# Performance work log

Measured on AMD Instinct MI355X. Metric: run time of the kernel, lower is better.

Reference implementation:

```python
import jax, jax.numpy as jnp
import numpy as np

B, S, E, H = 1, 2048, 512, 8
D = E // H
N = B * S
WIN_HALF = 32  # attention_window 64 -> +/-32
ALPHA = 0.1
LN_EPS = 1e-12
NEG_INF = -1e9


def _build_window_edges():
    # windowed graph: dst i attends to src j with |i-j| <= WIN_HALF, within each batch block
    i = np.arange(S)
    offs = np.arange(-WIN_HALF, WIN_HALF + 1)
    src = i[:, None] + offs[None, :]
    dst = np.broadcast_to(i[:, None], src.shape)
    valid = (src >= 0) & (src < S)
    src, dst = src[valid], dst[valid]
    srcs, dsts = [], []
    for b in range(B):
        srcs.append(src + b * S)
        dsts.append(dst + b * S)
    return (np.concatenate(srcs).astype(np.int32),
            np.concatenate(dsts).astype(np.int32))


def setup_inputs() -> dict:
    key = jax.random.key(0)
    ks = jax.random.split(key, 12)
    sc = 1.0 / np.sqrt(E)
    src_np, dst_np = _build_window_edges()
    return {
        "hidden_states": jax.random.normal(ks[0], (B, S, E), dtype=jnp.float32),
        "attention_mask": jnp.zeros((B, S), dtype=jnp.float32),
        "edge_src": jnp.asarray(src_np),
        "edge_dst": jnp.asarray(dst_np),
        "Wq": jax.random.normal(ks[1], (E, E), dtype=jnp.float32) * sc,
        "bq": jnp.zeros((E,), dtype=jnp.float32),
        "Wk": jax.random.normal(ks[2], (E, E), dtype=jnp.float32) * sc,
        "bk": jnp.zeros((E,), dtype=jnp.float32),
        "Wv": jax.random.normal(ks[3], (E, E), dtype=jnp.float32) * sc,
        "bv": jnp.zeros((E,), dtype=jnp.float32),
        "Wo": jax.random.normal(ks[4], (E, E), dtype=jnp.float32) * sc,
        "bo": jnp.zeros((E,), dtype=jnp.float32),
        "ln_g": jnp.ones((E,), dtype=jnp.float32),
        "ln_b": jnp.zeros((E,), dtype=jnp.float32),
    }


def reference(hidden_states, attention_mask, edge_src, edge_dst,
              Wq, bq, Wk, bk, Wv, bv, Wo, bo, ln_g, ln_b):
    x = hidden_states  # (B,S,E); node ordering n = b*S + s (matches torch reshape)
    q = ((x @ Wq + bq) / jnp.sqrt(jnp.asarray(D, x.dtype))).reshape(N, H, D)
    k = (x @ Wk + bk).reshape(N, H, D)
    v = (x @ Wv + bv).reshape(N, H, D)

    mask = (attention_mask >= 0).reshape(N)  # bool per node

    # u_dot_v('k','q','score'): per-edge, per-head dot product
    score = jnp.einsum('ehd,ehd->eh', k[edge_src], q[edge_dst])  # (Eg,H)
    score = jnp.where(mask[edge_src][:, None], score, NEG_INF)

    # edge_softmax over incoming edges of each destination node
    smax = jax.ops.segment_max(score, edge_dst, num_segments=N)
    p = jnp.exp(score - smax[edge_dst])
    denom = jax.ops.segment_sum(p, edge_dst, num_segments=N)
    p = p / denom[edge_dst]  # (Eg,H)

    # 5 diffusion steps: h <- A h, blended with residual v (dropout off in eval)
    h = v
    for _ in range(5):
        m = h[edge_src] * p[:, :, None]                      # u_mul_e
        h = jax.ops.segment_sum(m, edge_dst, num_segments=N)  # sum('m','h')
        h = (1.0 - ALPHA) * h + ALPHA * v

    attn = h.reshape(B, S, E)

    # DiffuserSelfOutput: dense -> residual add -> LayerNorm
    y = attn @ Wo + bo + hidden_states
    mu = y.mean(-1, keepdims=True)
    var = ((y - mu) ** 2).mean(-1, keepdims=True)
    out = (y - mu) * jax.lax.rsqrt(var + LN_EPS) * ln_g + ln_b
    return out
```

## Files before the change

kernel.cpp:

```cpp
#include <hip/hip_runtime.h>
#include <math.h>

#define S_LEN 2048
#define E_DIM 512
#define NE (S_LEN * E_DIM)
#define H_NUM 8
#define WH 32
#define NOFF 65
#define PROW (H_NUM * NOFF)
#define PN (S_LEN * PROW)

typedef float f32x4 __attribute__((ext_vector_type(4)));
typedef short short8 __attribute__((ext_vector_type(8)));

__device__ __forceinline__ unsigned short f2bf(float f) {
    union { float f; unsigned u; } cv; cv.f = f;
    unsigned u = cv.u;
    u += 0x7fffu + ((u >> 16) & 1u);
    return (unsigned short)(u >> 16);
}
__device__ __forceinline__ unsigned pk2(float x, float y) {
    return (unsigned)f2bf(x) | ((unsigned)f2bf(y) << 16);
}

#define LGKM_BARRIER() do {                                   \
    __builtin_amdgcn_sched_barrier(0);                        \
    asm volatile("s_waitcnt lgkmcnt(0)" ::: "memory");        \
    __builtin_amdgcn_s_barrier();                             \
    __builtin_amdgcn_sched_barrier(0);                        \
} while (0)

__device__ __forceinline__ void mfma_gemm_f32(
    const float* __restrict__ A, const float* __restrict__ W,
    const float* __restrict__ bias, float* __restrict__ C,
    float scale, int m0, int n0)
{
    __shared__ unsigned short As[2][64 * 40];
    __shared__ unsigned short Bs[2][64 * 40];
    const int tid = threadIdx.x;
    const int lane = tid & 63, wave = tid >> 6;
    const int quad = lane >> 4, l16 = lane & 15;
    const int wr = (wave >> 1) * 32, wc = (wave & 1) * 32;
    const int ar = tid >> 2, ac = (tid & 3) * 8;
    const int bn = tid & 63, bk0 = (tid >> 6) * 8;

    f32x4 acc00 = {0.f,0.f,0.f,0.f}, acc01 = acc00, acc10 = acc00, acc11 = acc00;

    const float* Arow = A + (size_t)(m0 + ar) * E_DIM;

    float4 a0r[2], a1r[2];
    float  br[2][8];

#define QLOAD(s_, i_) do {                                                    \
        int kk_ = (i_) * 32;                                                  \
        a0r[s_] = *(const float4*)(Arow + kk_ + ac);                          \
        a1r[s_] = *(const float4*)(Arow + kk_ + ac + 4);                      \
        _Pragma("unroll")                                                     \
        for (int j_ = 0; j_ < 8; ++j_)                                        \
            br[s_][j_] = W[(size_t)(kk_ + bk0 + j_) * E_DIM + n0 + bn];       \
    } while (0)

#define QPACK(s_, b_) do {                                                    \
        uint4 ap_;                                                            \
        ap_.x = pk2(a0r[s_].x, a0r[s_].y); ap_.y = pk2(a0r[s_].z, a0r[s_].w); \
        ap_.z = pk2(a1r[s_].x, a1r[s_].y); ap_.w = pk2(a1r[s_].z, a1r[s_].w); \
        *(uint4*)(&As[b_][0] + ar * 40 + ac) = ap_;                           \
        uint4 bp_;                                                            \
        bp_.x = pk2(br[s_][0], br[s_][1]); bp_.y = pk2(br[s_][2], br[s_][3]); \
        bp_.z = pk2(br[s_][4], br[s_][5]); bp_.w = pk2(br[s_][6], br[s_][7]); \
        *(uint4*)(&Bs[b_][0] + bn * 40 + bk0) = bp_;                          \
    } while (0)

    QLOAD(0, 0);
    QPACK(0, 0);
    QLOAD(1, 1);
    LGKM_BARRIER();

#pragma unroll
    for (int it = 0; it < 16; ++it) {
        if (it < 14) QLOAD(it & 1, it + 2);

        const unsigned short* Ab = &As[it & 1][0];
        const unsigned short* Bb = &Bs[it & 1][0];
        short8 fa0 = *(const short8*)(Ab + (wr + l16) * 40 + quad * 8);
        short8 fa1 = *(const short8*)(Ab + (wr + 16 + l16) * 40 + quad * 8);
        short8 fb0 = *(const short8*)(Bb + (wc + l16) * 40 + quad * 8);
        short8 fb1 = *(const short8*)(Bb + (wc + 16 + l16) * 40 + quad * 8);
        acc00 = __builtin_amdgcn_mfma_f32_16x16x32_bf16(fa0, fb0, acc00, 0, 0, 0);
        acc01 = __builtin_amdgcn_mfma_f32_16x16x32_bf16(fa0, fb1, acc01, 0, 0, 0);
        acc10 = __builtin_amdgcn_mfma_f32_16x16x32_bf16(fa1, fb0, acc10, 0, 0, 0);
        acc11 = __builtin_amdgcn_mfma_f32_16x16x32_bf16(fa1, fb1, acc11, 0, 0, 0);

        if (it < 15) {
            QPACK((it + 1) & 1, (it + 1) & 1);
            LGKM_BARRIER();
        }
    }
#undef QLOAD
#undef QPACK

#pragma unroll
    for (int mi = 0; mi < 2; ++mi) {
#pragma unroll
        for (int ni = 0; ni < 2; ++ni) {
            f32x4 a = (mi == 0) ? ((ni == 0) ? acc00 : acc01)
                                : ((ni == 0) ? acc10 : acc11);
            int n = n0 + wc + ni * 16 + l16;
            float bval = bias[n];
#pragma unroll
            for (int r = 0; r < 4; ++r) {
                int m = m0 + wr + mi * 16 + quad * 4 + r;
                C[(size_t)m * E_DIM + n] = (a[r] + bval) * scale;
            }
        }
    }
}

__global__ __launch_bounds__(256)
void qkv_gemm(const float* __restrict__ x,
              const float* __restrict__ Wq, const float* __restrict__ bq,
              const float* __restrict__ Wk, const float* __restrict__ bk,
              const float* __restrict__ Wv, const float* __restrict__ bv,
              float* __restrict__ q, float* __restrict__ k, float* __restrict__ v)
{
    const float* W; const float* b; float* o; float sc;
    if (blockIdx.z == 0)      { W = Wq; b = bq; o = q; sc = 0.125f; }
    else if (blockIdx.z == 1) { W = Wk; b = bk; o = k; sc = 1.0f; }
    else                      { W = Wv; b = bv; o = v; sc = 1.0f; }
    mfma_gemm_f32(x, W, b, o, sc, blockIdx.y * 64, blockIdx.x * 64);
}

#define SDN 32
__global__ __launch_bounds__(256)
void scores_d1(const float* __restrict__ q, const float* __restrict__ k,
               const float* __restrict__ v, const float* __restrict__ amask,
               unsigned short* __restrict__ Pb, unsigned short* __restrict__ hAb)
{
    const int i0 = blockIdx.x * SDN;
    const int h  = blockIdx.y;
    const int tid = threadIdx.x;
    __shared__ float ks[96 * 68];
    __shared__ float am[96];
    __shared__ float ps[SDN * NOFF];

    for (int e = tid; e < 96 * 16; e += 256) {
        int lr = e >> 4, c4 = e & 15;
        int j = i0 - WH + lr;
        int jc = min(max(j, 0), S_LEN - 1);
        *(float4*)(ks + lr * 68 + c4 * 4) =
            *(const float4*)(k + (size_t)jc * E_DIM + h * 64 + c4 * 4);
    }
    if (tid < 96) {
        int j = i0 - WH + tid;
        am[tid] = (j >= 0 && j < S_LEN) ? amask[j] : -1.0f;
    }

    const int dst = tid >> 3;
    const int og  = tid & 7;
    float4 qreg[16];
    {
        const float4* qrow = (const float4*)(q + (size_t)(i0 + dst) * E_DIM + h * 64);
#pragma unroll
        for (int t = 0; t < 16; ++t) qreg[t] = qrow[t];
    }
    __syncthreads();

    float sreg[9];
#pragma unroll
    for (int t = 0; t < 9; ++t) sreg[t] = -INFINITY;
#pragma unroll
    for (int t = 0; t < 9; ++t) {
        int off = og + 8 * t;
        if (off > 64) break;
        int j = i0 + dst + off - WH;
        if (j >= 0 && j < S_LEN) {
            int lr = dst + off;
            const float4* kr = (const float4*)(ks + lr * 68);
            float acc = 0.f;
#pragma unroll
            for (int u = 0; u < 16; ++u) {
                float4 a = qreg[u], bb = kr[u];
                acc += a.x * bb.x + a.y * bb.y + a.z * bb.z + a.w * bb.w;
            }
            sreg[t] = (am[lr] >= 0.f) ? acc : -1e9f;
        }
    }
    __syncthreads();

    for (int e = tid; e < 96 * 16; e += 256) {
        int lr = e >> 4, c4 = e & 15;
        int j = i0 - WH + lr;
        int jc = min(max(j, 0), S_LEN - 1);
        *(float4*)(ks + lr * 68 + c4 * 4) =
            *(const float4*)(v + (size_t)jc * E_DIM + h * 64 + c4 * 4);
    }

    float mx = sreg[0];
#pragma unroll
    for (int t = 1; t < 9; ++t) mx = fmaxf(mx, sreg[t]);
#pragma unroll
    for (int o = 1; o < 8; o <<= 1) mx = fmaxf(mx, __shfl_xor(mx, o, 64));
    float dn = 0.f;
#pragma unroll
    for (int t = 0; t < 9; ++t) {
        sreg[t] = expf(sreg[t] - mx);
        dn += sreg[t];
    }
#pragma unroll
    for (int o = 1; o < 8; o <<= 1) dn += __shfl_xor(dn, o, 64);
    float rinv = 1.f / dn;
#pragma unroll
    for (int t = 0; t < 9; ++t) {
        int off = og + 8 * t;
        if (off > 64) break;
        float pv = sreg[t] * rinv;
        Pb[(size_t)(i0 + dst) * PROW + h * NOFF + off] = f2bf(pv);
        ps[dst * NOFF + off] = pv;
    }
    __syncthreads();

    {
        const int ci = tid & 15;
        const int ob = (tid >> 4) * 2;
        float4 a0 = {0,0,0,0}, a1 = a0;
        for (int lr = ob; lr < ob + 66; ++lr) {
            float4 hval = *(const float4*)(ks + lr * 68 + ci * 4);
            int o0 = lr - ob;
            if (o0 <= 64) {
                float p = ps[ob * NOFF + o0];
                a0.x += p * hval.x; a0.y += p * hval.y; a0.z += p * hval.z; a0.w += p * hval.w;
            }
            int o1 = o0 - 1;
            if ((unsigned)o1 <= 64u) {
                float p = ps[(ob + 1) * NOFF + o1];
                a1.x += p * hval.x; a1.y += p * hval.y; a1.z += p * hval.z; a1.w += p * hval.w;
            }
        }
#pragma unroll
        for (int r = 0; r < 2; ++r) {
            float4 a = r ? a1 : a0;
            float4 vv = *(const float4*)(ks + (WH + ob + r) * 68 + ci * 4);
            ushort4 o4;
            o4.x = f2bf(0.9f * a.x + 0.1f * vv.x);
            o4.y = f2bf(0.9f * a.y + 0.1f * vv.y);
            o4.z = f2bf(0.9f * a.z + 0.1f * vv.z);
            o4.w = f2bf(0.9f * a.w + 0.1f * vv.w);
            *(ushort4*)(hAb + (size_t)(i0 + ob + r) * E_DIM + h * 64 + ci * 4) = o4;
        }
    }
}

__global__ __launch_bounds__(512)
void diffuse4m(const unsigned short* __restrict__ hAb, const float* __restrict__ v,
               const unsigned short* __restrict__ Pb, unsigned short* __restrict__ h5b)
{
    __shared__ unsigned short inT[64 * 328];
    __shared__ unsigned short m1T[64 * 264];
    __shared__ unsigned short ps2[256 * 136];
    unsigned short* m2T = inT;
    unsigned short* m3T = m1T;
    const int i0 = blockIdx.x * 64;
    const int h  = blockIdx.y;
    const int c0 = h * 64;
    const int tid  = threadIdx.x;
    const int lane = tid & 63, wave = tid >> 6;
    const int quad = lane >> 4, l16 = lane & 15;

    for (int e = tid; e < 256 * 68; e += 512)
        ((unsigned*)ps2)[e] = 0u;

    for (int e = tid; e < 160 * 16; e += 512) {
        int rp = (e >> 4) * 2, c4 = (e & 15) * 4;
        int ja = min(max(i0 - 128 + rp,     0), S_LEN - 1);
        int jb = min(max(i0 - 128 + rp + 1, 0), S_LEN - 1);
        ushort4 ha = *(const ushort4*)(hAb + (size_t)ja * E_DIM + c0 + c4);
        ushort4 hb = *(const ushort4*)(hAb + (size_t)jb * E_DIM + c0 + c4);
        *(unsigned*)(inT + (c4 + 0) * 328 + rp) = (unsigned)ha.x | ((unsigned)hb.x << 16);
        *(unsigned*)(inT + (c4 + 1) * 328 + rp) = (unsigned)ha.y | ((unsigned)hb.y << 16);
        *(unsigned*)(inT + (c4 + 2) * 328 + rp) = (unsigned)ha.z | ((unsigned)hb.z << 16);
        *(unsigned*)(inT + (c4 + 3) * 328 + rp) = (unsigned)ha.w | ((unsigned)hb.w << 16);
    }
    __syncthreads();

    for (int it = 0; it < 32; ++it) {
        int row = wave + it * 8;
        int jc = min(max(i0 - 96 + row, 0), S_LEN - 1);
        const unsigned short* src = Pb + (size_t)jc * PROW + h * NOFF;
        unsigned short* dst = ps2 + row * 136 + 32 + (row & 7);
        dst[lane] = src[lane];
        if (lane == 0) dst[64] = src[64];
    }
    __syncthreads();

#define BAND_FA(roff_)                                                        \
    *(const short8*)(ps2 + (size_t)(m + (roff_)) * 136 + 32 +                 \
                     ((m + (roff_)) & 7) + (k0q - m))

#pragma unroll
    for (int uu = 0; uu < 4; ++uu) {
        int u = wave + uu * 8;
        int mtb = (u >> 1) * 16;
        int ntb = (u & 1) * 32;
        f32x4 a0 = {0.f,0.f,0.f,0.f}, a1 = a0;
        int ks0 = mtb >> 5;
        const int m = mtb + l16;
#pragma unroll
        for (int t = 0; t < 3; ++t) {
            int k0q = (ks0 + t) * 32 + quad * 8;
            short8 fa = BAND_FA(0);
            short8 fb0 = *(const short8*)(inT + (ntb + l16) * 328 + k0q);
            short8 fb1 = *(const short8*)(inT + (ntb + 16 + l16) * 328 + k0q);
            a0 = __builtin_amdgcn_mfma_f32_16x16x32_bf16(fa, fb0, a0, 0, 0, 0);
            a1 = __builtin_amdgcn_mfma_f32_16x16x32_bf16(fa, fb1, a1, 0, 0, 0);
        }
#pragma unroll
        for (int nt = 0; nt < 2; ++nt) {
            f32x4 a = nt ? a1 : a0;
            int n = ntb + nt * 16 + l16;
            float o[4];
#pragma unroll
            for (int r = 0; r < 4; ++r) {
                int gm = min(max(i0 - 96 + mtb + quad * 4 + r, 0), S_LEN - 1);
                o[r] = 0.9f * a[r] + 0.1f * v[(size_t)gm * E_DIM + c0 + n];
            }
            *(unsigned*)(m1T + n * 264 + mtb + quad * 4)     = pk2(o[0], o[1]);
            *(unsigned*)(m1T + n * 264 + mtb + quad * 4 + 2) = pk2(o[2], o[3]);
        }
    }
    __syncthreads();

#pragma unroll
    for (int uu = 0; uu < 3; ++uu) {
        int u = wave + uu * 8;
        int mtb = (u >> 1) * 16;
        int ntb = (u & 1) * 32;
        f32x4 a0 = {0.f,0.f,0.f,0.f}, a1 = a0;
        int ks0 = mtb >> 5;
        const int m = mtb + l16;
#pragma unroll
        for (int t = 0; t < 3; ++t) {
            int k0q = (ks0 + t) * 32 + quad * 8;
            short8 fa = BAND_FA(32);
            short8 fb0 = *(const short8*)(m1T + (ntb + l16) * 264 + k0q);
            short8 fb1 = *(const short8*)(m1T + (ntb + 16 + l16) * 264 + k0q);
            a0 = __builtin_amdgcn_mfma_f32_16x16x32_bf16(fa, fb0, a0, 0, 0, 0);
            a1 = __builtin_amdgcn_mfma_f32_16x16x32_bf16(fa, fb1, a1, 0, 0, 0);
        }
#pragma unroll
        for (int nt = 0; nt < 2; ++nt) {
            f32x4 a = nt ? a1 : a0;
            int n = ntb + nt * 16 + l16;
            float o[4];
#pragma unroll
            for (int r = 0; r < 4; ++r) {
                int gm = min(max(i0 - 64 + mtb + quad * 4 + r, 0), S_LEN - 1);
                o[r] = 0.9f * a[r] + 0.1f * v[(size_t)gm * E_DIM + c0 + n];
            }
            *(unsigned*)(m2T + n * 200 + mtb + quad * 4)     = pk2(o[0], o[1]);
            *(unsigned*)(m2T + n * 200 + mtb + quad * 4 + 2) = pk2(o[2], o[3]);
        }
    }
    __syncthreads();

#pragma unroll
    for (int uu = 0; uu < 2; ++uu) {
        int u = wave + uu * 8;
        int mtb = (u >> 1) * 16;
        int ntb = (u & 1) * 32;
        f32x4 a0 = {0.f,0.f,0.f,0.f}, a1 = a0;
        int ks0 = mtb >> 5;
        const int m = mtb + l16;
#pragma unroll
        for (int t = 0; t < 3; ++t) {
            int k0q = (ks0 + t) * 32 + quad * 8;
            short8 fa = BAND_FA(64);
            short8 fb0 = *(const short8*)(m2T + (ntb + l16) * 200 + k0q);
            short8 fb1 = *(const short8*)(m2T + (ntb + 16 + l16) * 200 + k0q);
            a0 = __builtin_amdgcn_mfma_f32_16x16x32_bf16(fa, fb0, a0, 0, 0, 0);
            a1 = __builtin_amdgcn_mfma_f32_16x16x32_bf16(fa, fb1, a1, 0, 0, 0);
        }
#pragma unroll
        for (int nt = 0; nt < 2; ++nt) {
            f32x4 a = nt ? a1 : a0;
            int n = ntb + nt * 16 + l16;
            float o[4];
#pragma unroll
            for (int r = 0; r < 4; ++r) {
                int gm = min(max(i0 - 32 + mtb + quad * 4 + r, 0), S_LEN - 1);
                o[r] = 0.9f * a[r] + 0.1f * v[(size_t)gm * E_DIM + c0 + n];
            }
            *(unsigned*)(m3T + n * 136 + mtb + quad * 4)     = pk2(o[0], o[1]);
            *(unsigned*)(m3T + n * 136 + mtb + quad * 4 + 2) = pk2(o[2], o[3]);
        }
    }
    __syncthreads();

    {
        int u = wave;
        int mtb = (u >> 1) * 16;
        int ntb = (u & 1) * 32;
        f32x4 a0 = {0.f,0.f,0.f,0.f}, a1 = a0;
        int ks0 = mtb >> 5;
        const int m = mtb + l16;
#pragma unroll
        for (int t = 0; t < 3; ++t) {
            int k0q = (ks0 + t) * 32 + quad * 8;
            short8 fa = BAND_FA(96);
            short8 fb0 = *(const short8*)(m3T + (ntb + l16) * 136 + k0q);
            short8 fb1 = *(const short8*)(m3T + (ntb + 16 + l16) * 136 + k0q);
            a0 = __builtin_amdgcn_mfma_f32_16x16x32_bf16(fa, fb0, a0, 0, 0, 0);
            a1 = __builtin_amdgcn_mfma_f32_16x16x32_bf16(fa, fb1, a1, 0, 0, 0);
        }
#pragma unroll
        for (int nt = 0; nt < 2; ++nt) {
            f32x4 a = nt ? a1 : a0;
            int n = ntb + nt * 16 + l16;
#pragma unroll
            for (int r = 0; r < 4; ++r) {
                int gm = i0 + mtb + quad * 4 + r;
                float vv = v[(size_t)gm * E_DIM + c0 + n];
                h5b[(size_t)gm * E_DIM + c0 + n] = f2bf(0.9f * a[r] + 0.1f * vv);
            }
        }
    }
#undef BAND_FA
}

__global__ __launch_bounds__(512)
void oln5(const unsigned short* __restrict__ h5b, const float* __restrict__ Wo,
          const float* __restrict__ bo, const float* __restrict__ x,
          const float* __restrict__ g, const float* __restrict__ lb,
          float* __restrict__ out)
{
    __shared__ unsigned short Bs2[2][512 * 40];
    __shared__ float rsum[8][16], rsq[8][16];
    const int tid = threadIdx.x;
    const int lane = tid & 63, wave = tid >> 6;
    const int quad = lane >> 4, l16 = lane & 15;
    const int m0 = blockIdx.x * 16;
    const int n = tid;

    short8 far_[16];
#pragma unroll
    for (int t = 0; t < 16; ++t)
        far_[t] = *(const short8*)(h5b + (size_t)(m0 + l16) * E_DIM + t * 32 + quad * 8);

    {
        float w0[32];
#pragma unroll
        for (int j = 0; j < 32; ++j)
            w0[j] = Wo[(size_t)j * E_DIM + n];
#pragma unroll
        for (int t = 0; t < 4; ++t) {
            uint4 bp;
            bp.x = pk2(w0[t*8+0], w0[t*8+1]); bp.y = pk2(w0[t*8+2], w0[t*8+3]);
            bp.z = pk2(w0[t*8+4], w0[t*8+5]); bp.w = pk2(w0[t*8+6], w0[t*8+7]);
            *(uint4*)(&Bs2[0][0] + n * 40 + t * 8) = bp;
        }
    }
    LGKM_BARRIER();

    f32x4 acc[4];
#pragma unroll
    for (int t = 0; t < 4; ++t) acc[t] = (f32x4){0.f,0.f,0.f,0.f};

#pragma unroll
    for (int it = 0; it < 16; ++it) {
        float wn[32];
        if (it < 15) {
#pragma unroll
            for (int j = 0; j < 32; ++j)
                wn[j] = Wo[(size_t)((it + 1) * 32 + j) * E_DIM + n];
        }

#pragma unroll
        for (int nt = 0; nt < 4; ++nt) {
            short8 fb = *(const short8*)(&Bs2[it & 1][0] +
                                         (wave * 64 + nt * 16 + l16) * 40 + quad * 8);
            acc[nt] = __builtin_amdgcn_mfma_f32_16x16x32_bf16(far_[it], fb, acc[nt], 0, 0, 0);
        }

        if (it < 15) {
#pragma unroll
            for (int t = 0; t < 4; ++t) {
                uint4 bp;
                bp.x = pk2(wn[t*8+0], wn[t*8+1]); bp.y = pk2(wn[t*8+2], wn[t*8+3]);
                bp.z = pk2(wn[t*8+4], wn[t*8+5]); bp.w = pk2(wn[t*8+6], wn[t*8+7]);
                *(uint4*)(&Bs2[(it + 1) & 1][0] + n * 40 + t * 8) = bp;
            }
            LGKM_BARRIER();
        }
    }

    float s[4] = {0.f,0.f,0.f,0.f}, s2[4] = {0.f,0.f,0.f,0.f};
#pragma unroll
    for (int nt = 0; nt < 4; ++nt) {
        int nc = wave * 64 + nt * 16 + l16;
        float bv = bo[nc];
#pragma unroll
        for (int r = 0; r < 4; ++r) {
            int m = m0 + quad * 4 + r;
            float vl = acc[nt][r] + bv + x[(size_t)m * E_DIM + nc];
            acc[nt][r] = vl;
            s[r] += vl; s2[r] += vl * vl;
        }
    }
#pragma unroll
    for (int o = 1; o < 16; o <<= 1) {
#pragma unroll
        for (int r = 0; r < 4; ++r) {
            s[r]  += __shfl_xor(s[r], o, 64);
            s2[r] += __shfl_xor(s2[r], o, 64);
        }
    }
    if (l16 == 0) {
#pragma unroll
        for (int r = 0; r < 4; ++r) {
            rsum[wave][quad * 4 + r] = s[r];
            rsq[wave][quad * 4 + r]  = s2[r];
        }
    }
    __syncthreads();
    float mu[4], rs[4];
#pragma unroll
    for (int r = 0; r < 4; ++r) {
        int rl = quad * 4 + r;
        float tot = 0.f, tot2 = 0.f;
#pragma unroll
        for (int w = 0; w < 8; ++w) { tot += rsum[w][rl]; tot2 += rsq[w][rl]; }
        float m_ = tot * (1.f / 512.f);
        float var = tot2 * (1.f / 512.f) - m_ * m_;
        mu[r] = m_; rs[r] = rsqrtf(var + 1e-12f);
    }
#pragma unroll
    for (int nt = 0; nt < 4; ++nt) {
        int nc = wave * 64 + nt * 16 + l16;
        float gv = g[nc], bbv = lb[nc];
#pragma unroll
        for (int r = 0; r < 4; ++r) {
            int m = m0 + quad * 4 + r;
            out[(size_t)m * E_DIM + nc] = (acc[nt][r] - mu[r]) * rs[r] * gv + bbv;
        }
    }
}

extern "C" void kernel_launch(void* const* d_in, const int* in_sizes, int n_in,
                              void* d_out, int out_size, void* d_ws, size_t ws_size,
                              hipStream_t stream)
{
    const float* x     = (const float*)d_in[0];
    const float* amask = (const float*)d_in[1];
    const float* Wq = (const float*)d_in[4];
    const float* bq = (const float*)d_in[5];
    const float* Wk = (const float*)d_in[6];
    const float* bk = (const float*)d_in[7];
    const float* Wv = (const float*)d_in[8];
    const float* bv = (const float*)d_in[9];
    const float* Wo = (const float*)d_in[10];
    const float* bo = (const float*)d_in[11];
    const float* lng = (const float*)d_in[12];
    const float* lnb = (const float*)d_in[13];
    float* out = (float*)d_out;

    float* ws = (float*)d_ws;
    float* q  = ws;
    float* k  = ws + (size_t)NE;
    float* v  = ws + (size_t)2 * NE;
    unsigned short* Pb  = (unsigned short*)(ws + (size_t)3 * NE);
    unsigned short* hAb = Pb + (size_t)PN;
    unsigned short* h5b = hAb + (size_t)NE;

    qkv_gemm<<<dim3(8, 32, 3), 256, 0, stream>>>(x, Wq, bq, Wk, bk, Wv, bv, q, k, v);

    scores_d1<<<dim3(64, 8), 256, 0, stream>>>(q, k, v, amask, Pb, hAb);

    diffuse4m<<<dim3(32, 8), 512, 0, stream>>>(hAb, v, Pb, h5b);

    oln5<<<128, 512, 0, stream>>>(h5b, Wo, bo, x, lng, lnb, out);
}
```

Measured before the change: 155.1 us.

## Store V in bf16 and run first diffusion step on MFMA

The V projection is now written as bf16, which halves V traffic in the scores and diffusion kernels, and every consumer converts it back. The first diffusion step in scores_d1 moves from a scalar fp32 banded loop to bf16 MFMA. It uses a zero-padded, skewed bf16 probability tile and a transposed V tile in shared memory, so V is loaded up front and one barrier is removed. The cost is reduced precision of V and of step-1 probabilities, plus extra shared-memory setup.

```diff
diff --git a/kernel.cpp b/kernel.cpp
--- a/kernel.cpp
+++ b/kernel.cpp
@@ -22,6 +22,9 @@
 __device__ __forceinline__ unsigned pk2(float x, float y) {
     return (unsigned)f2bf(x) | ((unsigned)f2bf(y) << 16);
 }
+__device__ __forceinline__ float bf2f(unsigned short u) {
+    union { unsigned u; float f; } cv; cv.u = ((unsigned)u) << 16; return cv.f;
+}
 
 #define LGKM_BARRIER() do {                                   \
     __builtin_amdgcn_sched_barrier(0);                        \
@@ -33,7 +36,7 @@
 __device__ __forceinline__ void mfma_gemm_f32(
     const float* __restrict__ A, const float* __restrict__ W,
     const float* __restrict__ bias, float* __restrict__ C,
-    float scale, int m0, int n0)
+    unsigned short* __restrict__ Cb, float scale, int m0, int n0)
 {
     __shared__ unsigned short As[2][64 * 40];
     __shared__ unsigned short Bs[2][64 * 40];
@@ -110,7 +113,8 @@
 #pragma unroll
             for (int r = 0; r < 4; ++r) {
                 int m = m0 + wr + mi * 16 + quad * 4 + r;
-                C[(size_t)m * E_DIM + n] = (a[r] + bval) * scale;
+                if (Cb) Cb[(size_t)m * E_DIM + n] = f2bf((a[r] + bval) * scale);
+                else    C [(size_t)m * E_DIM + n] = (a[r] + bval) * scale;
             }
         }
     }
@@ -121,27 +125,35 @@
               const float* __restrict__ Wq, const float* __restrict__ bq,
               const float* __restrict__ Wk, const float* __restrict__ bk,
               const float* __restrict__ Wv, const float* __restrict__ bv,
-              float* __restrict__ q, float* __restrict__ k, float* __restrict__ v)
+              float* __restrict__ q, float* __restrict__ k,
+              unsigned short* __restrict__ vb)
 {
-    const float* W; const float* b; float* o; float sc;
-    if (blockIdx.z == 0)      { W = Wq; b = bq; o = q; sc = 0.125f; }
-    else if (blockIdx.z == 1) { W = Wk; b = bk; o = k; sc = 1.0f; }
-    else                      { W = Wv; b = bv; o = v; sc = 1.0f; }
-    mfma_gemm_f32(x, W, b, o, sc, blockIdx.y * 64, blockIdx.x * 64);
+    if (blockIdx.z == 0)
+        mfma_gemm_f32(x, Wq, bq, q, nullptr, 0.125f, blockIdx.y * 64, blockIdx.x * 64);
+    else if (blockIdx.z == 1)
+        mfma_gemm_f32(x, Wk, bk, k, nullptr, 1.0f, blockIdx.y * 64, blockIdx.x * 64);
+    else
+        mfma_gemm_f32(x, Wv, bv, nullptr, vb, 1.0f, blockIdx.y * 64, blockIdx.x * 64);
 }
 
 #define SDN 32
 __global__ __launch_bounds__(256)
 void scores_d1(const float* __restrict__ q, const float* __restrict__ k,
-               const float* __restrict__ v, const float* __restrict__ amask,
+               const unsigned short* __restrict__ vb, const float* __restrict__ amask,
                unsigned short* __restrict__ Pb, unsigned short* __restrict__ hAb)
 {
     const int i0 = blockIdx.x * SDN;
     const int h  = blockIdx.y;
     const int tid = threadIdx.x;
+    const int lane = tid & 63, wave = tid >> 6;
+    const int quad = lane >> 4, l16 = lane & 15;
     __shared__ float ks[96 * 68];
     __shared__ float am[96];
-    __shared__ float ps[SDN * NOFF];
+    __shared__ unsigned short vT[64 * 104];
+    __shared__ unsigned short psb[32 * 136];
+
+    for (int e = tid; e < 32 * 68; e += 256)
+        ((unsigned*)psb)[e] = 0u;
 
     for (int e = tid; e < 96 * 16; e += 256) {
         int lr = e >> 4, c4 = e & 15;
@@ -149,6 +161,17 @@
         int jc = min(max(j, 0), S_LEN - 1);
         *(float4*)(ks + lr * 68 + c4 * 4) =
             *(const float4*)(k + (size_t)jc * E_DIM + h * 64 + c4 * 4);
+    }
+    for (int e = tid; e < 48 * 16; e += 256) {
+        int rp = (e >> 4) * 2, c4 = (e & 15) * 4;
+        int ja = min(max(i0 - WH + rp,     0), S_LEN - 1);
+        int jb = min(max(i0 - WH + rp + 1, 0), S_LEN - 1);
+        ushort4 va = *(const ushort4*)(vb + (size_t)ja * E_DIM + h * 64 + c4);
+        ushort4 vc = *(const ushort4*)(vb + (size_t)jb * E_DIM + h * 64 + c4);
+        *(unsigned*)(vT + (c4 + 0) * 104 + rp) = (unsigned)va.x | ((unsigned)vc.x << 16);
+        *(unsigned*)(vT + (c4 + 1) * 104 + rp) = (unsigned)va.y | ((unsigned)vc.y << 16);
+        *(unsigned*)(vT + (c4 + 2) * 104 + rp) = (unsigned)va.z | ((unsigned)vc.z << 16);
+        *(unsigned*)(vT + (c4 + 3) * 104 + rp) = (unsigned)va.w | ((unsigned)vc.w << 16);
     }
     if (tid < 96) {
         int j = i0 - WH + tid;
@@ -185,15 +208,6 @@
             sreg[t] = (am[lr] >= 0.f) ? acc : -1e9f;
         }
     }
-    __syncthreads();
-
-    for (int e = tid; e < 96 * 16; e += 256) {
-        int lr = e >> 4, c4 = e & 15;
-        int j = i0 - WH + lr;
-        int jc = min(max(j, 0), S_LEN - 1);
-        *(float4*)(ks + lr * 68 + c4 * 4) =
-            *(const float4*)(v + (size_t)jc * E_DIM + h * 64 + c4 * 4);
-    }
 
     float mx = sreg[0];
 #pragma unroll
@@ -213,45 +227,39 @@
     for (int t = 0; t < 9; ++t) {
         int off = og + 8 * t;
         if (off > 64) break;
-        float pv = sreg[t] * rinv;
-        Pb[(size_t)(i0 + dst) * PROW + h * NOFF + off] = f2bf(pv);
-        ps[dst * NOFF + off] = pv;
-    }
-    __syncthreads();
-
-    {
-        const int ci = tid & 15;
-        const int ob = (tid >> 4) * 2;
-        float4 a0 = {0,0,0,0}, a1 = a0;
-        for (int lr = ob; lr < ob + 66; ++lr) {
-            float4 hval = *(const float4*)(ks + lr * 68 + ci * 4);
-            int o0 = lr - ob;
-            if (o0 <= 64) {
-                float p = ps[ob * NOFF + o0];
-                a0.x += p * hval.x; a0.y += p * hval.y; a0.z += p * hval.z; a0.w += p * hval.w;
-            }
-            int o1 = o0 - 1;
-            if ((unsigned)o1 <= 64u) {
-                float p = ps[(ob + 1) * NOFF + o1];
-                a1.x += p * hval.x; a1.y += p * hval.y; a1.z += p * hval.z; a1.w += p * hval.w;
-            }
-        }
-#pragma unroll
-        for (int r = 0; r < 2; ++r) {
-            float4 a = r ? a1 : a0;
-            float4 vv = *(const float4*)(ks + (WH + ob + r) * 68 + ci * 4);
-            ushort4 o4;
-            o4.x = f2bf(0.9f * a.x + 0.1f * vv.x);
-            o4.y = f2bf(0.9f * a.y + 0.1f * vv.y);
-            o4.z = f2bf(0.9f * a.z + 0.1f * vv.z);
-            o4.w = f2bf(0.9f * a.w + 0.1f * vv.w);
-            *(ushort4*)(hAb + (size_t)(i0 + ob + r) * E_DIM + h * 64 + ci * 4) = o4;
+        unsigned short pv16 = f2bf(sreg[t] * rinv);
+        Pb[(size_t)(i0 + dst) * PROW + h * NOFF + off] = pv16;
+        psb[dst * 136 + 32 + (dst & 7) + off] = pv16;
+    }
+    __syncthreads();
+
+#pragma unroll
+    for (int uu = 0; uu < 2; ++uu) {
+        int u = wave * 2 + uu;
+        int mtb = (u >> 2) * 16;
+        int ntb = (u & 3) * 16;
+        const int m = mtb + l16;
+        f32x4 a0 = {0.f,0.f,0.f,0.f};
+#pragma unroll
+        for (int t = 0; t < 3; ++t) {
+            int k0q = t * 32 + quad * 8;
+            short8 fa = *(const short8*)(psb + m * 136 + 32 + (m & 7) + (k0q - m));
+            short8 fb = *(const short8*)(vT + (ntb + l16) * 104 + k0q);
+            a0 = __builtin_amdgcn_mfma_f32_16x16x32_bf16(fa, fb, a0, 0, 0, 0);
+        }
+#pragma unroll
+        for (int r = 0; r < 4; ++r) {
+            int grow = mtb + quad * 4 + r;
+            int gcol = ntb + l16;
+            float vv = bf2f(vT[gcol * 104 + WH + grow]);
+            float o = 0.9f * a0[r] + 0.1f * vv;
+            hAb[(size_t)(i0 + grow) * E_DIM + h * 64 + gcol] = f2bf(o);
         }
     }
 }
 
 __global__ __launch_bounds__(512)
-void diffuse4m(const unsigned short* __restrict__ hAb, const float* __restrict__ v,
+void diffuse4m(const unsigned short* __restrict__ hAb, const unsigned short* __restrict__ vb,
                const unsigned short* __restrict__ Pb, unsigned short* __restrict__ h5b)
 {
     __shared__ unsigned short inT[64 * 328];
@@ -321,7 +329,7 @@
 #pragma unroll
             for (int r = 0; r < 4; ++r) {
                 int gm = min(max(i0 - 96 + mtb + quad * 4 + r, 0), S_LEN - 1);
-                o[r] = 0.9f * a[r] + 0.1f * v[(size_t)gm * E_DIM + c0 + n];
+                o[r] = 0.9f * a[r] + 0.1f * bf2f(vb[(size_t)gm * E_DIM + c0 + n]);
             }
             *(unsigned*)(m1T + n * 264 + mtb + quad * 4)     = pk2(o[0], o[1]);
             *(unsigned*)(m1T + n * 264 + mtb + quad * 4 + 2) = pk2(o[2], o[3]);
@@ -354,7 +362,7 @@
 #pragma unroll
             for (int r = 0; r < 4; ++r) {
                 int gm = min(max(i0 - 64 + mtb + quad * 4 + r, 0), S_LEN - 1);
-                o[r] = 0.9f * a[r] + 0.1f * v[(size_t)gm * E_DIM + c0 + n];
+                o[r] = 0.9f * a[r] + 0.1f * bf2f(vb[(size_t)gm * E_DIM + c0 + n]);
             }
             *(unsigned*)(m2T + n * 200 + mtb + quad * 4)     = pk2(o[0], o[1]);
             *(unsigned*)(m2T + n * 200 + mtb + quad * 4 + 2) = pk2(o[2], o[3]);
@@ -387,7 +395,7 @@
 #pragma unroll
             for (int r = 0; r < 4; ++r) {
                 int gm = min(max(i0 - 32 + mtb + quad * 4 + r, 0), S_LEN - 1);
-                o[r] = 0.9f * a[r] + 0.1f * v[(size_t)gm * E_DIM + c0 + n];
+                o[r] = 0.9f * a[r] + 0.1f * bf2f(vb[(size_t)gm * E_DIM + c0 + n]);
             }
             *(unsigned*)(m3T + n * 136 + mtb + quad * 4)     = pk2(o[0], o[1]);
             *(unsigned*)(m3T + n * 136 + mtb + quad * 4 + 2) = pk2(o[2], o[3]);
@@ -418,7 +426,7 @@
 #pragma unroll
             for (int r = 0; r < 4; ++r) {
                 int gm = i0 + mtb + quad * 4 + r;
-                float vv = v[(size_t)gm * E_DIM + c0 + n];
+                float vv = bf2f(vb[(size_t)gm * E_DIM + c0 + n]);
                 h5b[(size_t)gm * E_DIM + c0 + n] = f2bf(0.9f * a[r] + 0.1f * vv);
             }
         }
@@ -565,16 +573,16 @@
     float* ws = (float*)d_ws;
     float* q  = ws;
     float* k  = ws + (size_t)NE;
-    float* v  = ws + (size_t)2 * NE;
-    unsigned short* Pb  = (unsigned short*)(ws + (size_t)3 * NE);
+    unsigned short* vb  = (unsigned short*)(ws + (size_t)2 * NE);
+    unsigned short* Pb  = vb + (size_t)NE;
     unsigned short* hAb = Pb + (size_t)PN;
     unsigned short* h5b = hAb + (size_t)NE;
 
-    qkv_gemm<<<dim3(8, 32, 3), 256, 0, stream>>>(x, Wq, bq, Wk, bk, Wv, bv, q, k, v);
-
-    scores_d1<<<dim3(64, 8), 256, 0, stream>>>(q, k, v, amask, Pb, hAb);
-
-    diffuse4m<<<dim3(32, 8), 512, 0, stream>>>(hAb, v, Pb, h5b);
+    qkv_gemm<<<dim3(8, 32, 3), 256, 0, stream>>>(x, Wq, bq, Wk, bk, Wv, bv, q, k, vb);
+
+    scores_d1<<<dim3(64, 8), 256, 0, stream>>>(q, k, vb, amask, Pb, hAb);
+
+    diffuse4m<<<dim3(32, 8), 512, 0, stream>>>(hAb, vb, Pb, h5b);
 
     oln5<<<128, 512, 0, stream>>>(h5b, Wo, bo, x, lng, lnb, out);
 }
```

Measured after the change: 152.6 us. About the same (-1.6%).
